# Optimization experiments

Hardware: AMD Instinct MI355X
Metric: run time of the kernel (lower is better)

The kernel has to match this reference:

```python
import jax, jax.numpy as jnp
import numpy as np

NUM_ROWS = 4096      # out_features
GROUP_COUNT = 32
GROUP_SIZE = 128     # in_features = GROUP_COUNT * GROUP_SIZE = 4096
CODEBOOK_SIZE = 16   # 4-bit codes


def setup_inputs() -> dict:
    key = jax.random.key(0)
    k1, k2, k3, k4 = jax.random.split(key, 4)
    x = jax.random.normal(k1, (2, 1024, GROUP_COUNT * GROUP_SIZE), dtype=jnp.float32)
    codebooks = jax.random.normal(k2, (NUM_ROWS, GROUP_COUNT, CODEBOOK_SIZE), dtype=jnp.float32)
    codes = jax.random.randint(k3, (NUM_ROWS, GROUP_COUNT, GROUP_SIZE), 0, CODEBOOK_SIZE, dtype=jnp.int32)
    bias = jax.random.normal(k4, (NUM_ROWS,), dtype=jnp.float32)
    return {"x": x, "codebooks": codebooks, "codes": codes, "bias": bias}


def _dequantize_weight(codes, codebooks):
    # codes: [R, G, S] int indices into last dim of codebooks [R, G, B]
    R, G, S = codes.shape
    W_hat = jnp.take_along_axis(codebooks, codes, axis=2)  # [R, G, S]
    return W_hat.reshape(R, G * S)  # [out_features, in_features]


def reference(x, codebooks, codes, bias):
    W = _dequantize_weight(codes, codebooks)           # [out, in]
    out = jnp.einsum("bsi,oi->bso", x, W) + bias       # F.linear
    return out
```

## Files before the change

kernel.cpp:

```cpp
#include <hip/hip_runtime.h>
#include <hip/hip_bf16.h>
#include <stdint.h>


#define M_DIM 2048
#define N_DIM 4096
#define K_DIM 4096

typedef __attribute__((ext_vector_type(4))) int i32x4;

__device__ __forceinline__ void async_load16(const void* g, void* l) {
    __builtin_amdgcn_global_load_lds(
        (const __attribute__((address_space(1))) uint32_t*)(uintptr_t)g,
        (__attribute__((address_space(3))) uint32_t*)(uint32_t)(uintptr_t)l,
        16, 0, 0);
}

__device__ __forceinline__ uint32_t pack4(int a, int b, int c, int d) {
    return (uint32_t)(a & 255) | ((uint32_t)(b & 255) << 8) |
           ((uint32_t)(c & 255) << 16) | ((uint32_t)(d & 255) << 24);
}

__device__ __forceinline__ int q8(float v, float inv) {
    return (int)rintf(v * inv);
}

__global__ __launch_bounds__(256) void prepass_q8(
    const float* __restrict__ cb,
    const int* __restrict__ codes,
    const float* __restrict__ x,
    uint32_t* __restrict__ wq,
    uint32_t* __restrict__ xq,
    float* __restrict__ sw,
    float* __restrict__ sx)
{
    __shared__ float scb[512];
    __shared__ float red[256];
    const int b = blockIdx.x, t = threadIdx.x;
    if (b < N_DIM) {
        const int o = b;
        const float c0 = cb[(size_t)o * 512 + t];
        const float c1 = cb[(size_t)o * 512 + 256 + t];
        scb[t] = c0; scb[t + 256] = c1;
        red[t] = fmaxf(fabsf(c0), fabsf(c1));
        __syncthreads();
        for (int s = 128; s > 0; s >>= 1) {
            if (t < s) red[t] = fmaxf(red[t], red[t + s]);
            __syncthreads();
        }
        const float amax = fmaxf(red[0], 1e-20f);
        const float inv = 127.0f / amax;
        if (t == 0) sw[o] = amax / 127.0f;
        const int* crow = codes + (size_t)o * K_DIM;
        uint32_t* orow = wq + (size_t)o * 1024;
#pragma unroll
        for (int i = 0; i < 4; ++i) {
            const int d = t + i * 256;
            const int4 c = *(const int4*)(crow + d * 4);
            const float* g = scb + (d >> 5) * 16;
            orow[d] = pack4(q8(g[c.x], inv), q8(g[c.y], inv),
                            q8(g[c.z], inv), q8(g[c.w], inv));
        }
    } else {
        const int m = b - N_DIM;
        const float* row = x + (size_t)m * K_DIM;
        float4 v[4];
        float am = 0.f;
#pragma unroll
        for (int i = 0; i < 4; ++i) {
            v[i] = *(const float4*)(row + (size_t)(t + i * 256) * 4);
            am = fmaxf(am, fmaxf(fmaxf(fabsf(v[i].x), fabsf(v[i].y)),
                                 fmaxf(fabsf(v[i].z), fabsf(v[i].w))));
        }
        red[t] = am;
        __syncthreads();
        for (int s = 128; s > 0; s >>= 1) {
            if (t < s) red[t] = fmaxf(red[t], red[t + s]);
            __syncthreads();
        }
        const float amax = fmaxf(red[0], 1e-20f);
        const float inv = 127.0f / amax;
        if (t == 0) sx[m] = amax / 127.0f;
        uint32_t* orow = xq + (size_t)m * 1024;
#pragma unroll
        for (int i = 0; i < 4; ++i)
            orow[t + i * 256] = pack4(q8(v[i].x, inv), q8(v[i].y, inv),
                                      q8(v[i].z, inv), q8(v[i].w, inv));
    }
}

__global__ __launch_bounds__(512, 4) void gemm_i8(
    const unsigned char* __restrict__ A,
    const unsigned char* __restrict__ B,
    const float* __restrict__ sx,
    const float* __restrict__ sw,
    const float* __restrict__ bias,
    float* __restrict__ C)
{
    __shared__ __align__(16) unsigned char smem[32768];
    unsigned char* As = smem;
    unsigned char* Bs = smem + 16384;

    const int tid  = threadIdx.x;
    const int w    = tid >> 6;
    const int lane = tid & 63;
    const int l15  = lane & 15;
    const int quad = lane >> 4;
    const int m0   = blockIdx.y * 128;
    const int n0   = blockIdx.x * 128;
    const int wk   = w >> 2;
    const int wm   = ((w >> 1) & 1) * 64;
    const int wn   = (w & 1) * 64;

    const int srow = tid >> 3;
    const int sc   = (tid & 7) ^ (srow & 7);
    const int scol = sc * 16;

    const unsigned char* gA0 = A + (size_t)(m0 +      srow) * K_DIM + scol;
    const unsigned char* gA1 = A + (size_t)(m0 + 64 + srow) * K_DIM + scol;
    const unsigned char* gB0 = B + (size_t)(n0 +      srow) * K_DIM + scol;
    const unsigned char* gB1 = B + (size_t)(n0 + 64 + srow) * K_DIM + scol;

    unsigned char* lA0 = As +        w * 1024;
    unsigned char* lA1 = As + 8192 + w * 1024;
    unsigned char* lB0 = Bs +        w * 1024;
    unsigned char* lB1 = Bs + 8192 + w * 1024;

    const int fs = (((wk << 2) + quad) ^ (l15 & 7)) * 16;

    i32x4 acc[4][4] = {};

    for (int k0 = 0; k0 < K_DIM; k0 += 128) {
        async_load16(gA0 + k0, lA0);
        async_load16(gA1 + k0, lA1);
        async_load16(gB0 + k0, lB0);
        async_load16(gB1 + k0, lB1);
        __syncthreads();

        i32x4 af[4], bfr[4];
#pragma unroll
        for (int i = 0; i < 4; ++i) {
            af[i]  = *(const i32x4*)(As + (wm + i * 16 + l15) * 128 + fs);
            bfr[i] = *(const i32x4*)(Bs + (wn + i * 16 + l15) * 128 + fs);
        }
#pragma unroll
        for (int mi = 0; mi < 4; ++mi)
#pragma unroll
            for (int ni = 0; ni < 4; ++ni)
                acc[mi][ni] = __builtin_amdgcn_mfma_i32_16x16x64_i8(
                    af[mi], bfr[ni], acc[mi][ni], 0, 0, 0);
        __syncthreads();
    }

    int* red = (int*)smem;
    if (w == 4 || w == 5) {
        int* dst = red + (w & 1) * 4096;
#pragma unroll
        for (int mi = 0; mi < 4; ++mi)
#pragma unroll
            for (int ni = 0; ni < 4; ++ni)
#pragma unroll
                for (int r = 0; r < 4; ++r)
                    dst[(((mi * 4 + ni) * 4) + r) * 64 + lane] = acc[mi][ni][r];
    }
    __syncthreads();
    if (w == 0 || w == 1) {
        const int* src = red + (w & 1) * 4096;
#pragma unroll
        for (int mi = 0; mi < 4; ++mi)
#pragma unroll
            for (int ni = 0; ni < 4; ++ni)
#pragma unroll
                for (int r = 0; r < 4; ++r)
                    acc[mi][ni][r] += src[(((mi * 4 + ni) * 4) + r) * 64 + lane];
    }
    __syncthreads();
    if (w == 6 || w == 7) {
        int* dst = red + (w & 1) * 4096;
#pragma unroll
        for (int mi = 0; mi < 4; ++mi)
#pragma unroll
            for (int ni = 0; ni < 4; ++ni)
#pragma unroll
                for (int r = 0; r < 4; ++r)
                    dst[(((mi * 4 + ni) * 4) + r) * 64 + lane] = acc[mi][ni][r];
    }
    __syncthreads();
    if (w == 2 || w == 3) {
        const int* src = red + (w & 1) * 4096;
#pragma unroll
        for (int mi = 0; mi < 4; ++mi)
#pragma unroll
            for (int ni = 0; ni < 4; ++ni)
#pragma unroll
                for (int r = 0; r < 4; ++r)
                    acc[mi][ni][r] += src[(((mi * 4 + ni) * 4) + r) * 64 + lane];
    }

    if (w < 4) {
        float sxv[4][4], swv[4], bv[4];
#pragma unroll
        for (int mi = 0; mi < 4; ++mi)
#pragma unroll
            for (int r = 0; r < 4; ++r)
                sxv[mi][r] = sx[m0 + wm + mi * 16 + quad * 4 + r];
#pragma unroll
        for (int ni = 0; ni < 4; ++ni) {
            const int col = n0 + wn + ni * 16 + l15;
            swv[ni] = sw[col];
            bv[ni]  = bias[col];
        }
#pragma unroll
        for (int mi = 0; mi < 4; ++mi) {
#pragma unroll
            for (int ni = 0; ni < 4; ++ni) {
                const int col = n0 + wn + ni * 16 + l15;
                float* cp = C + (size_t)(m0 + wm + mi * 16 + quad * 4) * N_DIM + col;
#pragma unroll
                for (int r = 0; r < 4; ++r)
                    cp[(size_t)r * N_DIM] =
                        (float)acc[mi][ni][r] * (sxv[mi][r] * swv[ni]) + bv[ni];
            }
        }
    }
}

__global__ __launch_bounds__(256) void naive_kernel(
    const float* __restrict__ x, const float* __restrict__ cb,
    const int* __restrict__ codes, const float* __restrict__ bias,
    float* __restrict__ out)
{
    const size_t idx = (size_t)blockIdx.x * 256 + threadIdx.x;
    const int n = (int)(idx & 4095);
    const int m = (int)(idx >> 12);
    const float* xr = x + (size_t)m * K_DIM;
    float s = bias[n];
    for (int g = 0; g < 32; ++g) {
        const float* cbr = cb + ((size_t)n * 32 + g) * 16;
        const int* cr = codes + ((size_t)n * 32 + g) * 128;
        const float* xg = xr + g * 128;
        for (int ss = 0; ss < 128; ++ss) s += xg[ss] * cbr[cr[ss]];
    }
    out[idx] = s;
}

extern "C" void kernel_launch(void* const* d_in, const int* in_sizes, int n_in,
                              void* d_out, int out_size, void* d_ws, size_t ws_size,
                              hipStream_t stream) {
    const float* x     = (const float*)d_in[0];
    const float* cb    = (const float*)d_in[1];
    const int*   codes = (const int*)d_in[2];
    const float* bias  = (const float*)d_in[3];
    float* out = (float*)d_out;

    const size_t szW = (size_t)N_DIM * K_DIM;
    const size_t szX = (size_t)M_DIM * K_DIM;
    const size_t need = szW + szX + (N_DIM + M_DIM) * sizeof(float);

    if (ws_size >= need) {
        unsigned char* Wq = (unsigned char*)d_ws;
        unsigned char* Xq = Wq + szW;
        float* sw = (float*)(Xq + szX);
        float* sx = sw + N_DIM;
        prepass_q8<<<dim3(N_DIM + M_DIM), dim3(256), 0, stream>>>(
            cb, codes, x, (uint32_t*)Wq, (uint32_t*)Xq, sw, sx);
        gemm_i8<<<dim3(N_DIM / 128, M_DIM / 128), dim3(512), 0, stream>>>(
            Xq, Wq, sx, sw, bias, out);
    } else {
        naive_kernel<<<dim3((M_DIM * N_DIM) / 256), dim3(256), 0, stream>>>(x, cb, codes, bias, out);
    }
}
```

Before: 169.7 us.

## Double-buffer LDS tiles in int8 GEMM to overlap global loads with MFMA

Replaces the single-buffered load-sync-compute loop with a two-stage ping-pong LDS pipeline. The next K tile is issued via async global-to-LDS loads before the current tile's MFMAs run, with manual vmcnt waits and raw s_barrier calls. The aim is to hide global memory latency behind compute. LDS use doubles to 64KB per block, which may cut occupancy below the launch_bounds target of 4 blocks per CU.

```diff
diff --git a/kernel.cpp b/kernel.cpp
--- a/kernel.cpp
+++ b/kernel.cpp
@@ -89,6 +89,26 @@
     }
 }
 
+
+__device__ __forceinline__ void compute_tile(
+    const unsigned char* As, const unsigned char* Bs,
+    const int wm, const int wn, const int l15, const int fs,
+    i32x4 acc[4][4])
+{
+    i32x4 af[4], bfr[4];
+#pragma unroll
+    for (int i = 0; i < 4; ++i) {
+        af[i]  = *(const i32x4*)(As + (wm + i * 16 + l15) * 128 + fs);
+        bfr[i] = *(const i32x4*)(Bs + (wn + i * 16 + l15) * 128 + fs);
+    }
+#pragma unroll
+    for (int mi = 0; mi < 4; ++mi)
+#pragma unroll
+        for (int ni = 0; ni < 4; ++ni)
+            acc[mi][ni] = __builtin_amdgcn_mfma_i32_16x16x64_i8(
+                af[mi], bfr[ni], acc[mi][ni], 0, 0, 0);
+}
+
 __global__ __launch_bounds__(512, 4) void gemm_i8(
     const unsigned char* __restrict__ A,
     const unsigned char* __restrict__ B,
@@ -97,9 +117,11 @@
     const float* __restrict__ bias,
     float* __restrict__ C)
 {
-    __shared__ __align__(16) unsigned char smem[32768];
-    unsigned char* As = smem;
-    unsigned char* Bs = smem + 16384;
+    __shared__ __align__(16) unsigned char smem[65536];
+    unsigned char* As0 = smem;
+    unsigned char* Bs0 = smem + 16384;
+    unsigned char* As1 = smem + 32768;
+    unsigned char* Bs1 = smem + 49152;
 
     const int tid  = threadIdx.x;
     const int w    = tid >> 6;
@@ -121,35 +143,40 @@
     const unsigned char* gB0 = B + (size_t)(n0 +      srow) * K_DIM + scol;
     const unsigned char* gB1 = B + (size_t)(n0 + 64 + srow) * K_DIM + scol;
 
-    unsigned char* lA0 = As +        w * 1024;
-    unsigned char* lA1 = As + 8192 + w * 1024;
-    unsigned char* lB0 = Bs +        w * 1024;
-    unsigned char* lB1 = Bs + 8192 + w * 1024;
-
     const int fs = (((wk << 2) + quad) ^ (l15 & 7)) * 16;
 
+    auto stage = [&](unsigned char* As, unsigned char* Bs, int k) {
+        async_load16(gA0 + k, As +        w * 1024);
+        async_load16(gA1 + k, As + 8192 + w * 1024);
+        async_load16(gB0 + k, Bs +        w * 1024);
+        async_load16(gB1 + k, Bs + 8192 + w * 1024);
+    };
+
     i32x4 acc[4][4] = {};
 
-    for (int k0 = 0; k0 < K_DIM; k0 += 128) {
-        async_load16(gA0 + k0, lA0);
-        async_load16(gA1 + k0, lA1);
-        async_load16(gB0 + k0, lB0);
-        async_load16(gB1 + k0, lB1);
-        __syncthreads();
-
-        i32x4 af[4], bfr[4];
-#pragma unroll
-        for (int i = 0; i < 4; ++i) {
-            af[i]  = *(const i32x4*)(As + (wm + i * 16 + l15) * 128 + fs);
-            bfr[i] = *(const i32x4*)(Bs + (wn + i * 16 + l15) * 128 + fs);
-        }
-#pragma unroll
-        for (int mi = 0; mi < 4; ++mi)
-#pragma unroll
-            for (int ni = 0; ni < 4; ++ni)
-                acc[mi][ni] = __builtin_amdgcn_mfma_i32_16x16x64_i8(
-                    af[mi], bfr[ni], acc[mi][ni], 0, 0, 0);
-        __syncthreads();
+    stage(As0, Bs0, 0);
+    for (int k0 = 0; k0 < K_DIM; k0 += 256) {
+        stage(As1, Bs1, k0 + 128);
+        asm volatile("s_waitcnt vmcnt(4)" ::: "memory");
+        __builtin_amdgcn_s_barrier();
+        asm volatile("" ::: "memory");
+        compute_tile(As0, Bs0, wm, wn, l15, fs, acc);
+        asm volatile("s_waitcnt lgkmcnt(0)" ::: "memory");
+        __builtin_amdgcn_sched_barrier(0);
+        __builtin_amdgcn_s_barrier();
+
+        if (k0 + 256 < K_DIM) {
+            stage(As0, Bs0, k0 + 256);
+            asm volatile("s_waitcnt vmcnt(4)" ::: "memory");
+        } else {
+            asm volatile("s_waitcnt vmcnt(0)" ::: "memory");
+        }
+        __builtin_amdgcn_s_barrier();
+        asm volatile("" ::: "memory");
+        compute_tile(As1, Bs1, wm, wn, l15, fs, acc);
+        asm volatile("s_waitcnt lgkmcnt(0)" ::: "memory");
+        __builtin_amdgcn_sched_barrier(0);
+        __builtin_amdgcn_s_barrier();
     }
 
     int* red = (int*)smem;
```

After: 172.8 us. No clear change (+1.8%).
